# Kernel tuning notes

Measured on AMD Instinct MI355X. Metric: run time of the kernel, lower is better.

## Reference

```python
import jax, jax.numpy as jnp
import numpy as np


def _bit_reversal_perm(N, num_stages):
    idx = np.arange(N)
    perm = np.zeros(N, dtype=np.int64)
    for _ in range(num_stages):
        perm = (perm << 1) | (idx & 1)
        idx >>= 1
    return perm


def setup_inputs() -> dict:
    key = jax.random.key(0)
    k1, k2 = jax.random.split(key)
    B, N = 4096, 4096
    return {
        "x_re": jax.random.normal(k1, (B, N), dtype=jnp.float32),
        "x_im": jax.random.normal(k2, (B, N), dtype=jnp.float32),
    }


def reference(x_re, x_im):
    # Radix-2 DIT FFT, identical math to HollywoodFFT.forward.
    N = x_re.shape[-1]
    num_stages = int(round(np.log2(N)))
    batch = x_re.shape[:-1]

    # Input permutation is pure wiring: bit-reversal gather.
    perm = jnp.asarray(_bit_reversal_perm(N, num_stages))
    y_re = x_re[..., perm]
    y_im = x_im[..., perm]

    # Twiddle tile: W_N^k = exp(-2*pi*i*k/N) (precomputed constants).
    k = np.arange(N)
    ang = -2.0 * np.pi * k / N
    W_re_all = np.cos(ang).astype(np.float32)
    W_im_all = np.sin(ang).astype(np.float32)

    for s in range(num_stages):  # fixed small loop over log2(N) stages
        stride = 1 << s
        group_size = stride << 1
        # twiddle_idx = j * (N // group_size) for j in [0, stride), same for every group
        tw = np.arange(stride) * (N // group_size)
        W_re = jnp.asarray(W_re_all[tw])  # (stride,)
        W_im = jnp.asarray(W_im_all[tw])

        # (..., N) -> (..., N//group_size, 2, stride): [...,g,0,j]=upper, [...,g,1,j]=lower
        yr = y_re.reshape(*batch, N // group_size, 2, stride)
        yi = y_im.reshape(*batch, N // group_size, 2, stride)
        a_re, b_re = yr[..., 0, :], yr[..., 1, :]
        a_im, b_im = yi[..., 0, :], yi[..., 1, :]

        wb_re = W_re * b_re - W_im * b_im
        wb_im = W_re * b_im + W_im * b_re

        y_re = jnp.stack([a_re + wb_re, a_re - wb_re], axis=-2).reshape(*batch, N)
        y_im = jnp.stack([a_im + wb_im, a_im - wb_im], axis=-2).reshape(*batch, N)

    return y_re, y_im
```

## Files before the change

kernel.cpp:

```cpp
#include <hip/hip_runtime.h>


#define NFFT 4096

typedef float fvec4 __attribute__((ext_vector_type(4)));

__device__ __forceinline__ void fft16(float xr[16], float xi[16]) {
    const int br[16] = {0,8,4,12,2,10,6,14,1,9,5,13,3,11,7,15};
    float yr[16], yi[16];
#pragma unroll
    for (int j = 0; j < 16; ++j) { yr[j] = xr[br[j]]; yi[j] = xi[br[j]]; }
    const float W16r[8] = { 1.0f,  0.92387953251128675613f,  0.70710678118654752440f,
                            0.38268343236508977173f,  0.0f, -0.38268343236508977173f,
                           -0.70710678118654752440f, -0.92387953251128675613f };
    const float W16i[8] = { 0.0f, -0.38268343236508977173f, -0.70710678118654752440f,
                           -0.92387953251128675613f, -1.0f, -0.92387953251128675613f,
                           -0.70710678118654752440f, -0.38268343236508977173f };
#pragma unroll
    for (int s = 0; s < 4; ++s) {
        const int stride = 1 << s;
        const int tm = 8 >> s;
#pragma unroll
        for (int g = 0; g < 16; g += 2 * stride) {
#pragma unroll
            for (int p = 0; p < stride; ++p) {
                const int i0 = g + p, i1 = i0 + stride;
                const float twr = W16r[p * tm], twi = W16i[p * tm];
                const float brr = yr[i1] * twr - yi[i1] * twi;
                const float bii = yr[i1] * twi + yi[i1] * twr;
                const float ar = yr[i0], ai = yi[i0];
                yr[i0] = ar + brr; yi[i0] = ai + bii;
                yr[i1] = ar - brr; yi[i1] = ai - bii;
            }
        }
    }
#pragma unroll
    for (int j = 0; j < 16; ++j) { xr[j] = yr[j]; xi[j] = yi[j]; }
}

__global__ __launch_bounds__(256, 5)
void HollywoodFFT_53584011985637_kernel(const float* __restrict__ xre,
                                        const float* __restrict__ xim,
                                        float* __restrict__ outre,
                                        float* __restrict__ outim) {
    __shared__ __align__(16) float lr[NFFT];
    __shared__ __align__(16) float li[NFFT];

    const int t = threadIdx.x;
    const long long row = blockIdx.x;
    const float* __restrict__ xr_row = xre + row * NFFT;
    const float* __restrict__ xi_row = xim + row * NFFT;

    {
        const fvec4* __restrict__ xr4 = (const fvec4*)xr_row;
        const fvec4* __restrict__ xi4 = (const fvec4*)xi_row;
        fvec4 rr[4], ii[4];
#pragma unroll
        for (int q = 0; q < 4; ++q) { rr[q] = xr4[t + 256 * q]; ii[q] = xi4[t + 256 * q]; }
#pragma unroll
        for (int q = 0; q < 4; ++q) {
            ((fvec4*)lr)[t + 256 * q] = rr[q];
            ((fvec4*)li)[t + 256 * q] = ii[q];
        }
    }
    __syncthreads();

    float vr[16], vi[16];
    const int a = t & 15;
    const int u = t >> 4;

#pragma unroll
    for (int c = 0; c < 16; ++c) { vr[c] = lr[t + 256 * c]; vi[c] = li[t + 256 * c]; }
    fft16(vr, vi);
    __syncthreads();
#pragma unroll
    for (int uu = 0; uu < 16; ++uu) {
        const int id = a + 16 * ((t >> 4) ^ uu) + 256 * uu;
        lr[id] = vr[uu]; li[id] = vi[uu];
    }
    __syncthreads();

    {
        float s0, c0;
        __sincosf(-6.28318530717958647692f * (float)u * (1.0f / 256.0f), &s0, &c0);
        float twr = 1.0f, twi = 0.0f;
#pragma unroll
        for (int bb = 0; bb < 16; ++bb) {
            const int id = a + 16 * (bb ^ u) + 256 * u;
            const float rr = lr[id], ii = li[id];
            vr[bb] = rr * twr - ii * twi;
            vi[bb] = rr * twi + ii * twr;
            const float ntr = twr * c0 - twi * s0;
            twi = twr * s0 + twi * c0;
            twr = ntr;
        }
    }
    fft16(vr, vi);
    __syncthreads();
#pragma unroll
    for (int v = 0; v < 16; ++v) {
        const int id = (a ^ u) + 16 * (u ^ v) + 256 * v;
        lr[id] = vr[v]; li[id] = vi[v];
    }
    __syncthreads();

    const int u2 = t & 15, v2 = t >> 4;
    {
        float s0, c0;
        __sincosf(-6.28318530717958647692f * (float)(u2 + 16 * v2) * (1.0f / 4096.0f),
                  &s0, &c0);
        float twr = 1.0f, twi = 0.0f;
#pragma unroll
        for (int aa = 0; aa < 16; ++aa) {
            const int id = (aa ^ u2) + 16 * (u2 ^ v2) + 256 * v2;
            const float rr = lr[id], ii = li[id];
            vr[aa] = rr * twr - ii * twi;
            vi[aa] = rr * twi + ii * twr;
            const float ntr = twr * c0 - twi * s0;
            twi = twr * s0 + twi * c0;
            twr = ntr;
        }
    }
    fft16(vr, vi);
    __syncthreads();
#pragma unroll
    for (int w = 0; w < 16; ++w) {
        const int id = u2 + 16 * v2 + 256 * w;
        lr[id] = vr[w]; li[id] = vi[w];
    }
    __syncthreads();

    {
        float* __restrict__ or_row = outre + row * NFFT;
        float* __restrict__ oi_row = outim + row * NFFT;
#pragma unroll
        for (int q = 0; q < 4; ++q) {
            fvec4 rr = ((const fvec4*)lr)[t + 256 * q];
            fvec4 ii = ((const fvec4*)li)[t + 256 * q];
            __builtin_nontemporal_store(rr, (fvec4*)or_row + t + 256 * q);
            __builtin_nontemporal_store(ii, (fvec4*)oi_row + t + 256 * q);
        }
    }
}

extern "C" void kernel_launch(void* const* d_in, const int* in_sizes, int n_in,
                              void* d_out, int out_size, void* d_ws, size_t ws_size,
                              hipStream_t stream) {
    const float* xre = (const float*)d_in[0];
    const float* xim = (const float*)d_in[1];
    const int B = in_sizes[0] / NFFT;
    float* out = (float*)d_out;
    float* outre = out;
    float* outim = out + (size_t)B * NFFT;
    HollywoodFFT_53584011985637_kernel<<<dim3(B), dim3(256), 0, stream>>>(
        xre, xim, outre, outim);
}
```

Measured before the change: 235.4 us.

## Process several rows per block with register prefetch and direct final stores

Each block now handles multiple rows in a loop and loads the next row's input into registers while the current row's FFT runs, so global loads overlap with compute. Twiddle sincos values are computed once per thread instead of per row. The final LDS transpose and sync are dropped: the last radix-16 outputs go straight to global memory with scalar nontemporal stores. In exchange it uses more registers (launch bounds lowered to 4), the grid shrinks to 1024 blocks, and any remainder rows are silently skipped when B is not divisible by the grid size.

```diff
diff --git a/kernel.cpp b/kernel.cpp
--- a/kernel.cpp
+++ b/kernel.cpp
@@ -38,108 +38,110 @@
     for (int j = 0; j < 16; ++j) { xr[j] = yr[j]; xi[j] = yi[j]; }
 }
 
-__global__ __launch_bounds__(256, 5)
+__global__ __launch_bounds__(256, 4)
 void HollywoodFFT_53584011985637_kernel(const float* __restrict__ xre,
                                         const float* __restrict__ xim,
                                         float* __restrict__ outre,
-                                        float* __restrict__ outim) {
+                                        float* __restrict__ outim,
+                                        int rows_pb) {
     __shared__ __align__(16) float lr[NFFT];
     __shared__ __align__(16) float li[NFFT];
 
     const int t = threadIdx.x;
-    const long long row = blockIdx.x;
-    const float* __restrict__ xr_row = xre + row * NFFT;
-    const float* __restrict__ xi_row = xim + row * NFFT;
-
-    {
-        const fvec4* __restrict__ xr4 = (const fvec4*)xr_row;
-        const fvec4* __restrict__ xi4 = (const fvec4*)xi_row;
-        fvec4 rr[4], ii[4];
-#pragma unroll
-        for (int q = 0; q < 4; ++q) { rr[q] = xr4[t + 256 * q]; ii[q] = xi4[t + 256 * q]; }
-#pragma unroll
-        for (int q = 0; q < 4; ++q) {
-            ((fvec4*)lr)[t + 256 * q] = rr[q];
-            ((fvec4*)li)[t + 256 * q] = ii[q];
-        }
-    }
-    __syncthreads();
-
-    float vr[16], vi[16];
     const int a = t & 15;
     const int u = t >> 4;
 
+    float sB, cB, sC, cC;
+    __sincosf(-6.28318530717958647692f * (float)u * (1.0f / 256.0f), &sB, &cB);
+    __sincosf(-6.28318530717958647692f * (float)t * (1.0f / 4096.0f), &sC, &cC);
+
+    const long long row0 = (long long)blockIdx.x * rows_pb;
+
+    fvec4 pr[4], pim[4];
+    {
+        const fvec4* __restrict__ xr4 = (const fvec4*)(xre + row0 * NFFT);
+        const fvec4* __restrict__ xi4 = (const fvec4*)(xim + row0 * NFFT);
 #pragma unroll
-    for (int c = 0; c < 16; ++c) { vr[c] = lr[t + 256 * c]; vi[c] = li[t + 256 * c]; }
-    fft16(vr, vi);
-    __syncthreads();
-#pragma unroll
-    for (int uu = 0; uu < 16; ++uu) {
-        const int id = a + 16 * ((t >> 4) ^ uu) + 256 * uu;
-        lr[id] = vr[uu]; li[id] = vi[uu];
+        for (int q = 0; q < 4; ++q) { pr[q] = xr4[t + 256 * q]; pim[q] = xi4[t + 256 * q]; }
     }
-    __syncthreads();
 
-    {
-        float s0, c0;
-        __sincosf(-6.28318530717958647692f * (float)u * (1.0f / 256.0f), &s0, &c0);
-        float twr = 1.0f, twi = 0.0f;
-#pragma unroll
-        for (int bb = 0; bb < 16; ++bb) {
-            const int id = a + 16 * (bb ^ u) + 256 * u;
-            const float rr = lr[id], ii = li[id];
-            vr[bb] = rr * twr - ii * twi;
-            vi[bb] = rr * twi + ii * twr;
-            const float ntr = twr * c0 - twi * s0;
-            twi = twr * s0 + twi * c0;
-            twr = ntr;
-        }
-    }
-    fft16(vr, vi);
-    __syncthreads();
-#pragma unroll
-    for (int v = 0; v < 16; ++v) {
-        const int id = (a ^ u) + 16 * (u ^ v) + 256 * v;
-        lr[id] = vr[v]; li[id] = vi[v];
-    }
-    __syncthreads();
+    for (int i = 0; i < rows_pb; ++i) {
+        const long long row = row0 + i;
 
-    const int u2 = t & 15, v2 = t >> 4;
-    {
-        float s0, c0;
-        __sincosf(-6.28318530717958647692f * (float)(u2 + 16 * v2) * (1.0f / 4096.0f),
-                  &s0, &c0);
-        float twr = 1.0f, twi = 0.0f;
-#pragma unroll
-        for (int aa = 0; aa < 16; ++aa) {
-            const int id = (aa ^ u2) + 16 * (u2 ^ v2) + 256 * v2;
-            const float rr = lr[id], ii = li[id];
-            vr[aa] = rr * twr - ii * twi;
-            vi[aa] = rr * twi + ii * twr;
-            const float ntr = twr * c0 - twi * s0;
-            twi = twr * s0 + twi * c0;
-            twr = ntr;
-        }
-    }
-    fft16(vr, vi);
-    __syncthreads();
-#pragma unroll
-    for (int w = 0; w < 16; ++w) {
-        const int id = u2 + 16 * v2 + 256 * w;
-        lr[id] = vr[w]; li[id] = vi[w];
-    }
-    __syncthreads();
-
-    {
-        float* __restrict__ or_row = outre + row * NFFT;
-        float* __restrict__ oi_row = outim + row * NFFT;
 #pragma unroll
         for (int q = 0; q < 4; ++q) {
-            fvec4 rr = ((const fvec4*)lr)[t + 256 * q];
-            fvec4 ii = ((const fvec4*)li)[t + 256 * q];
-            __builtin_nontemporal_store(rr, (fvec4*)or_row + t + 256 * q);
-            __builtin_nontemporal_store(ii, (fvec4*)oi_row + t + 256 * q);
+            ((fvec4*)lr)[t + 256 * q] = pr[q];
+            ((fvec4*)li)[t + 256 * q] = pim[q];
         }
+        __syncthreads();
+
+        if (i + 1 < rows_pb) {
+            const fvec4* __restrict__ xr4 = (const fvec4*)(xre + (row + 1) * NFFT);
+            const fvec4* __restrict__ xi4 = (const fvec4*)(xim + (row + 1) * NFFT);
+#pragma unroll
+            for (int q = 0; q < 4; ++q) { pr[q] = xr4[t + 256 * q]; pim[q] = xi4[t + 256 * q]; }
+        }
+
+        float vr[16], vi[16];
+
+#pragma unroll
+        for (int c = 0; c < 16; ++c) { vr[c] = lr[t + 256 * c]; vi[c] = li[t + 256 * c]; }
+        fft16(vr, vi);
+        __syncthreads();
+#pragma unroll
+        for (int uu = 0; uu < 16; ++uu) {
+            const int id = a + 16 * ((t >> 4) ^ uu) + 256 * uu;
+            lr[id] = vr[uu]; li[id] = vi[uu];
+        }
+        __syncthreads();
+
+        {
+            float twr = 1.0f, twi = 0.0f;
+#pragma unroll
+            for (int bb = 0; bb < 16; ++bb) {
+                const int id = a + 16 * (bb ^ u) + 256 * u;
+                const float rr = lr[id], ii = li[id];
+                vr[bb] = rr * twr - ii * twi;
+                vi[bb] = rr * twi + ii * twr;
+                const float ntr = twr * cB - twi * sB;
+                twi = twr * sB + twi * cB;
+                twr = ntr;
+            }
+        }
+        fft16(vr, vi);
+        __syncthreads();
+#pragma unroll
+        for (int v = 0; v < 16; ++v) {
+            const int id = (a ^ u) + 16 * (u ^ v) + 256 * v;
+            lr[id] = vr[v]; li[id] = vi[v];
+        }
+        __syncthreads();
+
+        {
+            float twr = 1.0f, twi = 0.0f;
+#pragma unroll
+            for (int aa = 0; aa < 16; ++aa) {
+                const int id = (aa ^ a) + 16 * (a ^ u) + 256 * u;
+                const float rr = lr[id], ii = li[id];
+                vr[aa] = rr * twr - ii * twi;
+                vi[aa] = rr * twi + ii * twr;
+                const float ntr = twr * cC - twi * sC;
+                twi = twr * sC + twi * cC;
+                twr = ntr;
+            }
+        }
+        fft16(vr, vi);
+
+        {
+            float* __restrict__ or_row = outre + row * NFFT;
+            float* __restrict__ oi_row = outim + row * NFFT;
+#pragma unroll
+            for (int w = 0; w < 16; ++w) {
+                __builtin_nontemporal_store(vr[w], or_row + t + 256 * w);
+                __builtin_nontemporal_store(vi[w], oi_row + t + 256 * w);
+            }
+        }
+        __syncthreads();
     }
 }
 
@@ -152,6 +154,10 @@
     float* out = (float*)d_out;
     float* outre = out;
     float* outim = out + (size_t)B * NFFT;
-    HollywoodFFT_53584011985637_kernel<<<dim3(B), dim3(256), 0, stream>>>(
-        xre, xim, outre, outim);
+
+    int grid = 1024;
+    if (grid > B) grid = B;
+    const int rows_pb = B / grid;
+    HollywoodFFT_53584011985637_kernel<<<dim3(grid), dim3(256), 0, stream>>>(
+        xre, xim, outre, outim, rows_pb);
 }
```

New measurement: 327.3 us. 39.1% more time.
